# Optimization experiments

Hardware: AMD Instinct MI355X
Metric: run time of the kernel (lower is better)

The kernel has to match this reference:

```python
import jax, jax.numpy as jnp
import numpy as np

NUM_LEVELS = 1000
DIMENSIONS = 10000


def setup_inputs() -> dict:
    key = jax.random.key(0)
    k1, k2, k3, k4 = jax.random.split(key, 4)
    x = jax.random.uniform(k1, (32, 1, 28, 28), dtype=jnp.float32)  # MNIST-like, values in [0,1)
    # torchhd Random / Level hypervectors are +/-1 (MAP VSA)
    pos_weight = jnp.where(jax.random.normal(k2, (784, DIMENSIONS)) > 0, 1.0, -1.0).astype(jnp.float32)
    level_weight = jnp.where(jax.random.normal(k3, (NUM_LEVELS, DIMENSIONS)) > 0, 1.0, -1.0).astype(jnp.float32)
    classify_weight = jax.random.normal(k4, (10, DIMENSIONS), dtype=jnp.float32) * 0.01
    return {"x": x, "pos_weight": pos_weight, "level_weight": level_weight,
            "classify_weight": classify_weight}


def reference(x, pos_weight, level_weight, classify_weight):
    B = x.shape[0]
    xf = x.reshape(B, -1)  # flatten -> [B, 784]
    # Level embedding: quantize value in [0,1] to nearest of NUM_LEVELS indices
    idx = jnp.clip(jnp.round(xf * (NUM_LEVELS - 1)), 0, NUM_LEVELS - 1).astype(jnp.int32)
    levels = jnp.take(level_weight, idx, axis=0)  # [B, 784, D] gather
    # bind (elementwise mult with position HVs) + multiset (sum over pixels)
    hv = jnp.einsum('pd,bpd->bd', pos_weight, levels)  # [B, D]
    # hard_quantize: sign with 0 -> -1
    enc = jnp.where(hv > 0, 1.0, -1.0).astype(hv.dtype)
    logit = enc @ classify_weight.T  # [B, num_classes]
    return logit
```

## Files before the change

### kernel.cpp

```cpp
#include <hip/hip_runtime.h>
#include <stdint.h>

#define D    10000
#define P    784
#define B    32
#define NL   1000
#define NC   10

#define ROWW 320
#define ROWB (ROWW * 4)
#define NW   313
#define CHUNKS 8
#define PLEN  98
#define PLANES 7

#define OFFS_OFF  0
#define LVL_OFF   (B * P * 4)
#define POS_OFF   (LVL_OFF + NL * ROWB)
#define PART_OFF  (POS_OFF + P * ROWB)

#define PACK_BPR 10

__global__ void k_pack(const float* __restrict__ x,
                       const float* __restrict__ lvl, const float* __restrict__ pos,
                       int* __restrict__ offs,
                       uint32_t* __restrict__ lvl_b, uint32_t* __restrict__ pos_b,
                       float* __restrict__ out) {
    int bx  = blockIdx.x;
    int row = bx / PACK_BPR;
    int seg = bx % PACK_BPR;
    int d0  = seg * 1024 + threadIdx.x * 4;
    const float* src; uint32_t* dst;
    if (row < NL) { src = lvl + (size_t)row * D;        dst = lvl_b + (size_t)row * ROWW; }
    else          { src = pos + (size_t)(row - NL) * D; dst = pos_b + (size_t)(row - NL) * ROWW; }

    uint32_t nib = 0;
    if (d0 < D) {
        float4 v = *(const float4*)(src + d0);
        nib = (v.x < 0.0f ? 1u : 0u) | (v.y < 0.0f ? 2u : 0u) |
              (v.z < 0.0f ? 4u : 0u) | (v.w < 0.0f ? 8u : 0u);
    }
    int lane = threadIdx.x & 63;
    uint32_t val = nib << ((lane & 7) * 4);
    val |= __shfl_xor(val, 1, 64);
    val |= __shfl_xor(val, 2, 64);
    val |= __shfl_xor(val, 4, 64);
    if ((lane & 7) == 0) {
        int gword = (seg * 1024 + (threadIdx.x & ~7) * 4) >> 5;
        dst[gword] = val;
    }

    if (bx < 98) {
        int i = bx * 256 + threadIdx.x;
        float v = rintf(x[i] * 999.0f);
        v = fminf(fmaxf(v, 0.0f), 999.0f);
        offs[i] = (int)v * ROWB;
    }
    if (bx < 2) {
        int i = bx * 256 + threadIdx.x;
        if (i < B * NC) out[i] = 0.0f;
    }
}

template <int N>
__device__ inline void bsadd(const uint32_t* a, const uint32_t* b, uint32_t* s) {
    uint32_t cin = 0;
    #pragma unroll
    for (int k = 0; k < N; k++) {
        uint32_t t = a[k] ^ b[k];
        s[k] = t ^ cin;
        cin  = (a[k] & b[k]) | (cin & t);
    }
    s[N] = cin;
}

__global__ __launch_bounds__(512) void k_bindcls(const int* __restrict__ offs,
                                                 const uint32_t* __restrict__ lvl_b,
                                                 const uint32_t* __restrict__ pos_b,
                                                 const float* __restrict__ cw,
                                                 float* __restrict__ out) {
    int b = blockIdx.y, seg = blockIdx.x;
    int wave = threadIdx.x >> 6, lane = threadIdx.x & 63;
    int gw = seg * 64 + lane;
    const int* po = offs + b * P + wave * PLEN;
    const uint32_t* pb = pos_b + (size_t)(wave * PLEN) * ROWW + gw;
    const char* lb = (const char*)lvl_b;
    int wb = gw << 2;

    uint32_t pl[PLANES];
    #pragma unroll
    for (int k = 0; k < PLANES; k++) pl[k] = 0;

    #pragma unroll 7
    for (int i = 0; i < PLEN; i += 2) {
        int o0 = po[i], o1 = po[i + 1];
        uint32_t l0 = *(const uint32_t*)(lb + o0 + wb);
        uint32_t l1 = *(const uint32_t*)(lb + o1 + wb);
        uint32_t x0 = l0 ^ pb[(size_t)i * ROWW];
        uint32_t x1 = l1 ^ pb[(size_t)(i + 1) * ROWW];
        uint32_t t  = x0 ^ x1;
        uint32_t cr = (x0 & x1) | (pl[0] & t);
        pl[0] ^= t;
        #pragma unroll
        for (int k = 1; k < PLANES; k++) { uint32_t tt = pl[k] & cr; pl[k] ^= cr; cr = tt; }
    }

    __shared__ uint32_t red[CHUNKS][PLANES][64];
    #pragma unroll
    for (int k = 0; k < PLANES; k++) red[wave][k][lane] = pl[k];
    __syncthreads();

    __shared__ uint32_t minus_s[64];
    if (wave == 0) {
        uint32_t ch[CHUNKS][PLANES];
        #pragma unroll
        for (int c = 0; c < CHUNKS; c++)
            #pragma unroll
            for (int k = 0; k < PLANES; k++)
                ch[c][k] = red[c][k][lane];

        uint32_t s01[8], s23[8], s45[8], s67[8], t0[9], t1[9], s[10];
        bsadd<7>(ch[0], ch[1], s01);
        bsadd<7>(ch[2], ch[3], s23);
        bsadd<7>(ch[4], ch[5], s45);
        bsadd<7>(ch[6], ch[7], s67);
        bsadd<8>(s01, s23, t0);
        bsadd<8>(s45, s67, t1);
        bsadd<9>(t0, t1, s);
        minus_s[lane] = s[9] | (s[8] & s[7] & (s[3] | s[4] | s[5] | s[6]));
    }
    __syncthreads();

    if (wave < 5) {
        uint32_t minus = minus_s[lane];
        float sgn[32];
        #pragma unroll
        for (int j = 0; j < 32; j++) sgn[j] = ((minus >> j) & 1u) ? -1.0f : 1.0f;

        float a0 = 0.0f, a1 = 0.0f;
        int c0 = wave * 2;
        const float* r0 = cw + (size_t)c0 * D + gw * 32;
        const float* r1 = r0 + D;
        if (gw < NW - 1) {
            #pragma unroll
            for (int j = 0; j < 32; j++) { a0 = fmaf(sgn[j], r0[j], a0); a1 = fmaf(sgn[j], r1[j], a1); }
        } else if (gw == NW - 1) {
            #pragma unroll
            for (int j = 0; j < 16; j++) { a0 = fmaf(sgn[j], r0[j], a0); a1 = fmaf(sgn[j], r1[j], a1); }
        }
        for (int o = 32; o > 0; o >>= 1) { a0 += __shfl_down(a0, o, 64); a1 += __shfl_down(a1, o, 64); }
        if (lane == 0) {
            atomicAdd(out + b * NC + c0,     a0);
            atomicAdd(out + b * NC + c0 + 1, a1);
        }
    }
}

extern "C" void kernel_launch(void* const* d_in, const int* in_sizes, int n_in,
                              void* d_out, int out_size, void* d_ws, size_t ws_size,
                              hipStream_t stream) {
    const float* x   = (const float*)d_in[0];
    const float* pos = (const float*)d_in[1];
    const float* lvl = (const float*)d_in[2];
    const float* cw  = (const float*)d_in[3];
    float* out = (float*)d_out;

    char* ws = (char*)d_ws;
    int*       offs  = (int*)(ws + OFFS_OFF);
    uint32_t*  lvl_b = (uint32_t*)(ws + LVL_OFF);
    uint32_t*  pos_b = (uint32_t*)(ws + POS_OFF);

    k_pack   <<<dim3((NL + P) * PACK_BPR), 256, 0, stream>>>(x, lvl, pos, offs, lvl_b, pos_b, out);
    k_bindcls<<<dim3(5, B),                512, 0, stream>>>(offs, lvl_b, pos_b, cw, out);
}
```

Measured before the change: 114.2 us.

## Double waves per block in bind kernel and compute level offsets in shared memory

```diff
diff --git a/kernel.cpp b/kernel.cpp
--- a/kernel.cpp
+++ b/kernel.cpp
@@ -10,20 +10,17 @@
 #define ROWW 320
 #define ROWB (ROWW * 4)
 #define NW   313
-#define CHUNKS 8
-#define PLEN  98
-#define PLANES 7
 
-#define OFFS_OFF  0
-#define LVL_OFF   (B * P * 4)
-#define POS_OFF   (LVL_OFF + NL * ROWB)
-#define PART_OFF  (POS_OFF + P * ROWB)
+#define CHUNKS 16
+#define PLEN   49
+#define PLANES 6
+
+#define LVL_OFF  0
+#define POS_OFF  (NL * ROWB)
 
 #define PACK_BPR 10
 
-__global__ void k_pack(const float* __restrict__ x,
-                       const float* __restrict__ lvl, const float* __restrict__ pos,
-                       int* __restrict__ offs,
+__global__ void k_pack(const float* __restrict__ lvl, const float* __restrict__ pos,
                        uint32_t* __restrict__ lvl_b, uint32_t* __restrict__ pos_b,
                        float* __restrict__ out) {
     int bx  = blockIdx.x;
@@ -49,13 +46,6 @@
         int gword = (seg * 1024 + (threadIdx.x & ~7) * 4) >> 5;
         dst[gword] = val;
     }
-
-    if (bx < 98) {
-        int i = bx * 256 + threadIdx.x;
-        float v = rintf(x[i] * 999.0f);
-        v = fminf(fmaxf(v, 0.0f), 999.0f);
-        offs[i] = (int)v * ROWB;
-    }
     if (bx < 2) {
         int i = bx * 256 + threadIdx.x;
         if (i < B * NC) out[i] = 0.0f;
@@ -74,25 +64,39 @@
     s[N] = cin;
 }
 
-__global__ __launch_bounds__(512) void k_bindcls(const int* __restrict__ offs,
-                                                 const uint32_t* __restrict__ lvl_b,
-                                                 const uint32_t* __restrict__ pos_b,
-                                                 const float* __restrict__ cw,
-                                                 float* __restrict__ out) {
+__global__ __launch_bounds__(1024) void k_bindcls(const float* __restrict__ x,
+                                                  const uint32_t* __restrict__ lvl_b,
+                                                  const uint32_t* __restrict__ pos_b,
+                                                  const float* __restrict__ cw,
+                                                  float* __restrict__ out) {
     int b = blockIdx.y, seg = blockIdx.x;
-    int wave = threadIdx.x >> 6, lane = threadIdx.x & 63;
+    int tid  = threadIdx.x;
+    int wave = tid >> 6, lane = tid & 63;
     int gw = seg * 64 + lane;
-    const int* po = offs + b * P + wave * PLEN;
+
+    __shared__ int      offs_l[P];
+    __shared__ uint32_t red[CHUNKS][PLANES][64];
+    __shared__ uint32_t red2[4][8][64];
+    __shared__ uint32_t minus_s[64];
+
+    if (tid < P) {
+        float v = rintf(x[b * P + tid] * 999.0f);
+        v = fminf(fmaxf(v, 0.0f), 999.0f);
+        offs_l[tid] = (int)v * ROWB;
+    }
+    __syncthreads();
+
     const uint32_t* pb = pos_b + (size_t)(wave * PLEN) * ROWW + gw;
     const char* lb = (const char*)lvl_b;
     int wb = gw << 2;
+    const int* po = offs_l + wave * PLEN;
 
     uint32_t pl[PLANES];
     #pragma unroll
     for (int k = 0; k < PLANES; k++) pl[k] = 0;
 
-    #pragma unroll 7
-    for (int i = 0; i < PLEN; i += 2) {
+    #pragma unroll 8
+    for (int i = 0; i + 1 < PLEN; i += 2) {
         int o0 = po[i], o1 = po[i + 1];
         uint32_t l0 = *(const uint32_t*)(lb + o0 + wb);
         uint32_t l1 = *(const uint32_t*)(lb + o1 + wb);
@@ -104,28 +108,44 @@
         #pragma unroll
         for (int k = 1; k < PLANES; k++) { uint32_t tt = pl[k] & cr; pl[k] ^= cr; cr = tt; }
     }
+    {
+        int o0 = po[PLEN - 1];
+        uint32_t x0 = (*(const uint32_t*)(lb + o0 + wb)) ^ pb[(size_t)(PLEN - 1) * ROWW];
+        uint32_t cr = x0;
+        #pragma unroll
+        for (int k = 0; k < PLANES; k++) { uint32_t tt = pl[k] & cr; pl[k] ^= cr; cr = tt; }
+    }
 
-    __shared__ uint32_t red[CHUNKS][PLANES][64];
     #pragma unroll
     for (int k = 0; k < PLANES; k++) red[wave][k][lane] = pl[k];
     __syncthreads();
 
-    __shared__ uint32_t minus_s[64];
-    if (wave == 0) {
-        uint32_t ch[CHUNKS][PLANES];
+    if (wave < 4) {
+        uint32_t ch[4][PLANES];
         #pragma unroll
-        for (int c = 0; c < CHUNKS; c++)
+        for (int c = 0; c < 4; c++)
             #pragma unroll
             for (int k = 0; k < PLANES; k++)
-                ch[c][k] = red[c][k][lane];
+                ch[c][k] = red[wave * 4 + c][k][lane];
+        uint32_t b1[7], b2[7], p8[8];
+        bsadd<6>(ch[0], ch[1], b1);
+        bsadd<6>(ch[2], ch[3], b2);
+        bsadd<7>(b1, b2, p8);
+        #pragma unroll
+        for (int k = 0; k < 8; k++) red2[wave][k][lane] = p8[k];
+    }
+    __syncthreads();
 
-        uint32_t s01[8], s23[8], s45[8], s67[8], t0[9], t1[9], s[10];
-        bsadd<7>(ch[0], ch[1], s01);
-        bsadd<7>(ch[2], ch[3], s23);
-        bsadd<7>(ch[4], ch[5], s45);
-        bsadd<7>(ch[6], ch[7], s67);
-        bsadd<8>(s01, s23, t0);
-        bsadd<8>(s45, s67, t1);
+    if (wave == 0) {
+        uint32_t q[4][8];
+        #pragma unroll
+        for (int c = 0; c < 4; c++)
+            #pragma unroll
+            for (int k = 0; k < 8; k++)
+                q[c][k] = red2[c][k][lane];
+        uint32_t t0[9], t1[9], s[10];
+        bsadd<8>(q[0], q[1], t0);
+        bsadd<8>(q[2], q[3], t1);
         bsadd<9>(t0, t1, s);
         minus_s[lane] = s[9] | (s[8] & s[7] & (s[3] | s[4] | s[5] | s[6]));
     }
@@ -166,10 +186,9 @@
     float* out = (float*)d_out;
 
     char* ws = (char*)d_ws;
-    int*       offs  = (int*)(ws + OFFS_OFF);
     uint32_t*  lvl_b = (uint32_t*)(ws + LVL_OFF);
     uint32_t*  pos_b = (uint32_t*)(ws + POS_OFF);
 
-    k_pack   <<<dim3((NL + P) * PACK_BPR), 256, 0, stream>>>(x, lvl, pos, offs, lvl_b, pos_b, out);
-    k_bindcls<<<dim3(5, B),                512, 0, stream>>>(offs, lvl_b, pos_b, cw, out);
+    k_pack   <<<dim3((NL + P) * PACK_BPR), 256, 0, stream>>>(lvl, pos, lvl_b, pos_b, out);
+    k_bindcls<<<dim3(5, B),               1024, 0, stream>>>(x, lvl_b, pos_b, cw, out);
 }
```

After: 115.7 us. Within noise of the previous version (+1.3%).
